# Optimization experiments

Measured on AMD Instinct MI355X. Metric: run time of the kernel, lower is better.

The kernel has to match this reference:

```python
import jax, jax.numpy as jnp
import numpy as np

D = 1024          # input_dim
H = 16            # num_heads
S = 2             # scalar
MAX_LEN = 2048
HEAD_DIM = D // H // S      # 32
DV = D // H                 # 64, value head dim
SCALING = (D // H) ** -0.5


def setup_inputs() -> dict:
    key = jax.random.key(0)
    k1, k2, k3, k4, k5, k6 = jax.random.split(key, 6)
    L, B = 2046, 4
    input_tensor = jax.random.normal(k1, (L, B, D), dtype=jnp.float32)
    # k_v_proj: Linear(MAX_LEN, MAX_LEN // S); bias exists but is unused in forward
    w_kv = jax.random.normal(k2, (MAX_LEN // S, MAX_LEN), dtype=jnp.float32) / np.sqrt(MAX_LEN)
    # q_proj: Linear(D, D // S)
    w_q = jax.random.normal(k3, (D // S, D), dtype=jnp.float32) / np.sqrt(D)
    b_q = jax.random.normal(k4, (D // S,), dtype=jnp.float32) * 0.01
    # out_proj: Linear(D, D)
    w_out = jax.random.normal(k5, (D, D), dtype=jnp.float32) / np.sqrt(D)
    b_out = jax.random.normal(k6, (D,), dtype=jnp.float32) * 0.01
    return {"input_tensor": input_tensor, "w_kv": w_kv, "w_q": w_q,
            "b_q": b_q, "w_out": w_out, "b_out": b_out}


def reference(input_tensor, w_kv, w_q, b_q, w_out, b_out):
    L, B, _ = input_tensor.shape
    P = L // S + 1                       # projected (low-rank) sequence length
    X = jnp.transpose(input_tensor, (1, 0, 2))        # [B, L, D]
    q = X @ w_q.T + b_q                                # [B, L, D/S]
    Wp = w_kv.T[:L, :P]                                # [L, P] sequence projection
    v = jnp.einsum('bld,lp->bdp', X, Wp)               # [B, D, P]
    k = jnp.einsum('blc,lp->bcp', q, Wp)               # [B, D/S, P]
    q = q * SCALING
    # q: b l (h d) -> b h l d
    qh = q.reshape(B, L, H, HEAD_DIM).transpose(0, 2, 1, 3)
    # k: b (d h) p -> b h d p   (d outer, h inner in the channel split)
    kh = k.reshape(B, HEAD_DIM, H, P).transpose(0, 2, 1, 3)
    # v: b (d h) p -> b h p d
    vh = v.reshape(B, DV, H, P).transpose(0, 2, 3, 1)
    attn = jnp.einsum('bhld,bhdp->bhlp', qh, kh)       # [B, H, L, P]
    attn = jax.nn.softmax(attn.astype(jnp.float32), axis=-1).astype(attn.dtype)
    out = jnp.einsum('bhlp,bhpd->bhld', attn, vh)      # [B, H, L, DV]
    # (b h) l d -> b l (d h): d outer, h inner in concat
    out = out.transpose(0, 2, 3, 1).reshape(B, L, D)
    out = out @ w_out.T + b_out                        # [B, L, D]
    return jnp.transpose(out, (1, 0, 2))               # [L, B, D]
```

## Files before the change

kernel.cpp:

```cpp
#include <hip/hip_runtime.h>
#include <hip/hip_bf16.h>

typedef long long i64;
typedef unsigned int uint;
using u16 = unsigned short;
using f32x4  = __attribute__((ext_vector_type(4))) float;
using bf16x8 = __attribute__((ext_vector_type(8))) short;
using u32x4  = __attribute__((ext_vector_type(4))) uint;
using u16x4  = __attribute__((ext_vector_type(4))) u16;

#define QSCALE 0.18033688011112042f

#if __has_builtin(__builtin_amdgcn_exp2f)
#define EXP2(x) __builtin_amdgcn_exp2f(x)
#else
#define EXP2(x) __builtin_exp2f(x)
#endif

__device__ __forceinline__ u16 f2b(float x) {
    uint u = __float_as_uint(x);
    return (u16)((u + 0x7FFFu + ((u >> 16) & 1u)) >> 16);
}
__device__ __forceinline__ uint cvt_pk_bf16(float lo, float hi) {
    uint r;
    asm("v_cvt_pk_bf16_f32 %0, %1, %2" : "=v"(r) : "v"(lo), "v"(hi));
    return r;
}

__global__ __launch_bounds__(256) void conv_pad(
    const float* __restrict__ src, u16* __restrict__ dst,
    int M_valid, int K_valid, int kshift, int s_row)
{
    i64 i = (i64)blockIdx.x * 256 + threadIdx.x;
    int m = (int)(i >> (kshift - 2));
    int k = ((int)(i & ((1 << (kshift - 2)) - 1))) << 2;
    u16x4 hv;
    #pragma unroll
    for (int j = 0; j < 4; ++j) {
        int kk = k + j;
        float x = (m < M_valid && kk < K_valid) ? src[(i64)m * s_row + kk] : 0.f;
        hv[j] = f2b(x);
    }
    *(u16x4*)(dst + ((i64)m << kshift) + k) = hv;
}

__global__ __launch_bounds__(256) void conv_wout_perm(
    const float* __restrict__ w, u16* __restrict__ dst)
{
    int i = blockIdx.x * 256 + threadIdx.x;
    int n = i >> 8, kp4 = (i & 255) << 2;
    u16x4 hv;
    #pragma unroll
    for (int j = 0; j < 4; ++j) {
        int kp = kp4 + j;
        hv[j] = f2b(w[((i64)n << 10) + ((kp & 63) << 4) + (kp >> 6)]);
    }
    *(u16x4*)(dst + ((i64)n << 10) + kp4) = hv;
}

__global__ __launch_bounds__(256) void build_kvA(
    const float* __restrict__ X, const float* __restrict__ qp,
    u16* __restrict__ dst)
{
    const int b = blockIdx.z, r0 = blockIdx.y * 64, l0 = blockIdx.x * 64;
    const int tid = threadIdx.x;
    __shared__ float ts[64][65];
    #pragma unroll
    for (int t = 0; t < 16; ++t) {
        int idx = t * 256 + tid;
        int ch = idx & 63, lr = idx >> 6;
        int lg = l0 + lr;
        float v = 0.f;
        if (lg < 2046) {
            if (r0 < 1024) v = X[(i64)lg * 4096 + b * 1024 + (r0 + ch)];
            else           v = qp[((i64)lg * 4 + b) * 512 + (r0 - 1024 + ch)];
        }
        ts[lr][ch] = v;
    }
    __syncthreads();
    #pragma unroll
    for (int t = 0; t < 16; ++t) {
        int idx = t * 256 + tid;
        int ll = idx & 63, rl = idx >> 6;
        dst[((i64)b * 1536 + r0 + rl) * 2048 + l0 + ll] = f2b(ts[ll][rl]);
    }
}

template<int MODE>
__global__ __launch_bounds__(256) void gemm_bf16(
    const u16* __restrict__ A, i64 a_bs,
    const u16* __restrict__ Bm,
    float* __restrict__ C, const float* __restrict__ bias,
    u16* __restrict__ x0, u16* __restrict__ x1,
    int Krow, int KT, int M_valid)
{
    __shared__ __align__(16) u16 As[4096], Bs[4096];
    const int tid = threadIdx.x, lane = tid & 63, w = tid >> 6;
    const int fr = lane & 15, g = lane >> 4;
    const int nb = blockIdx.x, mb = blockIdx.y, bz = blockIdx.z;

    const u16* src = (w < 2)
        ? (A + (i64)bz * a_bs + ((i64)mb * 128 + (w & 1) * 64) * Krow)
        : (Bm + ((i64)nb * 128 + (w & 1) * 64) * Krow);
    u16* dstb = (w < 2) ? As : Bs;
    const int R0 = (w & 1) * 64;
    const int lr = lane >> 2, lcg = lane & 3;

    f32x4 acc[4][4];
    #pragma unroll
    for (int i = 0; i < 4; ++i)
        #pragma unroll
        for (int j = 0; j < 4; ++j)
            acc[i][j] = (f32x4){0.f, 0.f, 0.f, 0.f};

    u32x4 st[4];
    #pragma unroll
    for (int it = 0; it < 4; ++it)
        st[it] = *(const u32x4*)(src + (i64)(it * 16 + lr) * Krow + lcg * 8);

    const int wr = (w >> 1) * 64, wc = (w & 1) * 64;

    for (int kt = 0; kt < KT; ++kt) {
        __syncthreads();
        #pragma unroll
        for (int it = 0; it < 4; ++it) {
            int R = R0 + it * 16 + lr;
            *(u32x4*)((char*)dstb + R * 64 + ((lcg ^ (R & 3)) << 4)) = st[it];
        }
        __syncthreads();
        if (kt + 1 < KT) {
            #pragma unroll
            for (int it = 0; it < 4; ++it)
                st[it] = *(const u32x4*)(src + (i64)(it * 16 + lr) * Krow
                                             + (kt + 1) * 32 + lcg * 8);
        }
        bf16x8 ah[4], bh[4];
        #pragma unroll
        for (int mi = 0; mi < 4; ++mi) {
            int rr = wr + mi * 16 + fr;
            ah[mi] = *(const bf16x8*)((const char*)As + rr * 64 + ((g * 16) ^ ((rr & 3) << 4)));
        }
        #pragma unroll
        for (int ni = 0; ni < 4; ++ni) {
            int rr = wc + ni * 16 + fr;
            bh[ni] = *(const bf16x8*)((const char*)Bs + rr * 64 + ((g * 16) ^ ((rr & 3) << 4)));
        }
        #pragma unroll
        for (int mi = 0; mi < 4; ++mi)
            #pragma unroll
            for (int ni = 0; ni < 4; ++ni)
                acc[mi][ni] = __builtin_amdgcn_mfma_f32_16x16x32_bf16(
                    ah[mi], bh[ni], acc[mi][ni], 0, 0, 0);
    }

    #pragma unroll
    for (int mi = 0; mi < 4; ++mi)
        #pragma unroll
        for (int ni = 0; ni < 4; ++ni) {
            int gm0 = mb * 128 + wr + mi * 16 + g * 4;
            int gn  = nb * 128 + wc + ni * 16 + fr;
            #pragma unroll
            for (int r = 0; r < 4; ++r) {
                int gm = gm0 + r;
                float val = acc[mi][ni][r];
                if (MODE == 0) {
                    val += bias[gn];
                    C[(i64)gm * 512 + gn] = val;
                    x0[(i64)gm * 512 + gn] = f2b(val * QSCALE);
                } else if (MODE == 1) {
                    if (gm < 1024) {
                        int e = gm >> 4, hh = gm & 15;
                        i64 s = ((i64)(bz * 16 + hh) * 64 + e) * 1024
                              + (gn & ~31) + (((gn >> 2) & 3) << 3)
                              + (gn & 3) + (((gn >> 4) & 1) << 2);
                        x1[s] = f2b(val);
                    } else {
                        int c2 = gm - 1024, d = c2 >> 4, hh = c2 & 15;
                        x0[((i64)(bz * 16 + hh) * 1024 + gn) * 32 + d] = f2b(val);
                    }
                } else {
                    if (gm < M_valid)
                        C[(i64)bz * 1024 + (i64)gm * 4096 + gn] = val + bias[gn];
                }
            }
        }
}

__global__ __launch_bounds__(256) void attn_mfma(
    const u16* __restrict__ qb, const u16* __restrict__ kT,
    const u16* __restrict__ vT, u16* __restrict__ attA)
{
    const int g0 = blockIdx.x;
    const int xcd = g0 & 7, sub = g0 >> 3;
    const int lblk = sub & 15;
    const int bh = xcd + ((sub >> 4) << 3);
    const int b = bh >> 4, h = bh & 15;
    const int tid = threadIdx.x, lane = tid & 63, w = tid >> 6;
    const int fr = lane & 15, g = lane >> 4;
    const int l0 = lblk * 128 + w * 32;

    __shared__ __align__(16) u16 kbuf[2][2560];
    __shared__ __align__(16) u16 vbuf[2][4608];

    bf16x8 aq[2];
    #pragma unroll
    for (int mf = 0; mf < 2; ++mf)
        aq[mf] = *(const bf16x8*)(qb + ((i64)((l0 + mf * 16 + fr) * 4 + b) * 512
                                        + h * 32 + g * 8));

    const f32x4 zf = {0.f, 0.f, 0.f, 0.f};

    const int sr = tid >> 2, sc = tid & 3;
    const u16* ksrc = kT + (i64)bh * 32768 + sr * 32 + sc * 8;
    char* kdst = (char*)&kbuf[0][0] + sr * 80 + sc * 16;
    const u16* vsrc = vT + (i64)bh * 65536 + (i64)sr * 1024 + sc * 8;
    char* vdst = (char*)&vbuf[0][0] + sr * 144 + sc * 16;

    *(u32x4*)kdst = *(const u32x4*)ksrc;
    *(u32x4*)vdst = *(const u32x4*)vsrc;
    *(u32x4*)(vdst + 64) = *(const u32x4*)(vsrc + 32);
    __syncthreads();

    float l_part[2] = {0.f, 0.f};
    f32x4 o[2][4];
    #pragma unroll
    for (int mf = 0; mf < 2; ++mf)
        #pragma unroll
        for (int nf = 0; nf < 4; ++nf)
            o[mf][nf] = zf;

    for (int t = 0; t < 16; ++t) {
        const int cur = t & 1;
        const int tn = (t < 15) ? t + 1 : 15;

        u32x4 knx  = *(const u32x4*)(ksrc + tn * 2048);
        u32x4 vnx0 = *(const u32x4*)(vsrc + tn * 64);
        u32x4 vnx1 = *(const u32x4*)(vsrc + tn * 64 + 32);

        const char* kc_ = (const char*)&kbuf[cur][0];
        f32x4 s[2][4];
        __builtin_amdgcn_s_setprio(1);
        #pragma unroll
        for (int nf = 0; nf < 4; ++nf) {
            bf16x8 ak = *(const bf16x8*)(kc_ + (nf * 16 + fr) * 80 + g * 16);
            s[0][nf] = __builtin_amdgcn_mfma_f32_16x16x32_bf16(ak, aq[0], zf, 0, 0, 0);
            s[1][nf] = __builtin_amdgcn_mfma_f32_16x16x32_bf16(ak, aq[1], zf, 0, 0, 0);
        }
        __builtin_amdgcn_s_setprio(0);

        u32x4 ppk[2][2];
        #pragma unroll
        for (int mf = 0; mf < 2; ++mf)
            #pragma unroll
            for (int nf = 0; nf < 4; ++nf) {
                float p_[4];
                #pragma unroll
                for (int r = 0; r < 4; ++r) p_[r] = EXP2(s[mf][nf][r]);
                l_part[mf] += (p_[0] + p_[1]) + (p_[2] + p_[3]);
                ppk[mf][nf >> 1][(nf & 1) * 2 + 0] = cvt_pk_bf16(p_[0], p_[1]);
                ppk[mf][nf >> 1][(nf & 1) * 2 + 1] = cvt_pk_bf16(p_[2], p_[3]);
            }

        {
            const int nb_ = cur ^ 1;
            *(u32x4*)(kdst + nb_ * 5120) = knx;
            *(u32x4*)(vdst + nb_ * 9216) = vnx0;
            *(u32x4*)(vdst + nb_ * 9216 + 64) = vnx1;
        }

        const char* vc_ = (const char*)&vbuf[cur][0];
        __builtin_amdgcn_s_setprio(1);
        #pragma unroll
        for (int ks = 0; ks < 2; ++ks) {
            bf16x8 ap0 = __builtin_bit_cast(bf16x8, ppk[0][ks]);
            bf16x8 ap1 = __builtin_bit_cast(bf16x8, ppk[1][ks]);
            #pragma unroll
            for (int nf = 0; nf < 4; ++nf) {
                bf16x8 bv = *(const bf16x8*)(vc_ + (nf * 16 + fr) * 144
                                                 + ks * 64 + g * 16);
                o[0][nf] = __builtin_amdgcn_mfma_f32_16x16x32_bf16(ap0, bv, o[0][nf], 0, 0, 0);
                o[1][nf] = __builtin_amdgcn_mfma_f32_16x16x32_bf16(ap1, bv, o[1][nf], 0, 0, 0);
            }
        }
        __builtin_amdgcn_s_setprio(0);

        __syncthreads();
    }

    #pragma unroll
    for (int mf = 0; mf < 2; ++mf) {
        l_part[mf] += __shfl_xor(l_part[mf], 16);
        l_part[mf] += __shfl_xor(l_part[mf], 32);
    }
    #pragma unroll
    for (int mf = 0; mf < 2; ++mf)
        #pragma unroll
        for (int r = 0; r < 4; ++r) {
            int l = l0 + mf * 16 + g * 4 + r;
            float tot = __shfl(l_part[mf], g * 4 + r);
            if (l < 2046) {
                float inv = 1.f / tot;
                #pragma unroll
                for (int nf = 0; nf < 4; ++nf)
                    attA[((i64)b * 2048 + l) * 1024 + h * 64 + nf * 16 + fr]
                        = f2b(o[mf][nf][r] * inv);
            }
        }
}

extern "C" void kernel_launch(void* const* d_in, const int* in_sizes, int n_in,
                              void* d_out, int out_size, void* d_ws, size_t ws_size,
                              hipStream_t stream) {
    const float* input = (const float*)d_in[0];
    const float* w_kv  = (const float*)d_in[1];
    const float* w_q   = (const float*)d_in[2];
    const float* b_q   = (const float*)d_in[3];
    const float* w_out = (const float*)d_in[4];
    const float* b_out = (const float*)d_in[5];
    float* out = (float*)d_out;

    char* W = (char*)d_ws;
    float* qp    = (float*)(W + 0);
    u16* Xb      = (u16*)(W + 16777216);
    u16* qb      = (u16*)(W + 33554432);
    u16* wq_b    = (u16*)(W + 41943040);
    u16* wkv_b   = (u16*)(W + 42991616);
    u16* wout_b  = (u16*)(W + 47185920);
    u16* kvA     = (u16*)(W + 49283072);
    u16* kT      = (u16*)(W + 74448896);
    u16* vT      = (u16*)(W + 78643200);
    u16* attA    = (u16*)(W + 87031808);

    dim3 blk(256);

    conv_pad<<<8192, blk, 0, stream>>>(input, Xb, 8184, 1024, 10, 1024);
    conv_pad<<<512,  blk, 0, stream>>>(w_q, wq_b, 512, 1024, 10, 1024);
    conv_pad<<<2048, blk, 0, stream>>>(w_kv, wkv_b, 1024, 2046, 11, 2048);
    conv_wout_perm<<<1024, blk, 0, stream>>>(w_out, wout_b);

    gemm_bf16<0><<<dim3(4, 64, 1), blk, 0, stream>>>(
        Xb, 0, wq_b, qp, b_q, qb, nullptr, 1024, 32, 8192);

    build_kvA<<<dim3(32, 24, 4), blk, 0, stream>>>(input, qp, kvA);

    gemm_bf16<1><<<dim3(8, 12, 4), blk, 0, stream>>>(
        kvA, (i64)1536 * 2048, wkv_b, nullptr, nullptr, kT, vT, 2048, 64, 1536);

    attn_mfma<<<dim3(1024), blk, 0, stream>>>(qb, kT, vT, attA);

    gemm_bf16<2><<<dim3(8, 16, 4), blk, 0, stream>>>(
        attA, (i64)2048 * 1024, wout_b, out, b_out, nullptr, nullptr, 1024, 32, 2046);
}
```

Baseline: 195.2 us.

## Double GEMM K-tile, add XCD-aware block mapping, drop fp32 q buffer

The GEMM kernel now loads a 64-wide K slice per iteration with an 8-way XOR swizzle, which halves the loop trip count and barrier count. Blocks are remapped from a 1D grid so that neighbouring tiles land on the same XCD, aiming for better L2 reuse. The fp32 q projection output is removed: q is stored once in bf16 without the scale, the scale is applied inside the attention exp2, and build_kvA reads bf16 X and q instead of fp32. Together these cut global traffic and loop overhead, at the cost of double the LDS per block and more staging registers, which may lower occupancy. They also feed k from bf16-rounded q instead of fp32 q, a small precision change.

```diff
diff --git a/kernel.cpp b/kernel.cpp
--- a/kernel.cpp
+++ b/kernel.cpp
@@ -21,6 +21,9 @@
     uint u = __float_as_uint(x);
     return (u16)((u + 0x7FFFu + ((u >> 16) & 1u)) >> 16);
 }
+__device__ __forceinline__ float b2f(u16 h) {
+    return __uint_as_float((uint)h << 16);
+}
 __device__ __forceinline__ uint cvt_pk_bf16(float lo, float hi) {
     uint r;
     asm("v_cvt_pk_bf16_f32 %0, %1, %2" : "=v"(r) : "v"(lo), "v"(hi));
@@ -59,7 +62,7 @@
 }
 
 __global__ __launch_bounds__(256) void build_kvA(
-    const float* __restrict__ X, const float* __restrict__ qp,
+    const u16* __restrict__ Xb, const u16* __restrict__ qu,
     u16* __restrict__ dst)
 {
     const int b = blockIdx.z, r0 = blockIdx.y * 64, l0 = blockIdx.x * 64;
@@ -72,8 +75,8 @@
         int lg = l0 + lr;
         float v = 0.f;
         if (lg < 2046) {
-            if (r0 < 1024) v = X[(i64)lg * 4096 + b * 1024 + (r0 + ch)];
-            else           v = qp[((i64)lg * 4 + b) * 512 + (r0 - 1024 + ch)];
+            if (r0 < 1024) v = b2f(Xb[((i64)lg * 4 + b) * 1024 + (r0 + ch)]);
+            else           v = b2f(qu[((i64)lg * 4 + b) * 512 + (r0 - 1024 + ch)]);
         }
         ts[lr][ch] = v;
     }
@@ -94,17 +97,25 @@
     u16* __restrict__ x0, u16* __restrict__ x1,
     int Krow, int KT, int M_valid)
 {
-    __shared__ __align__(16) u16 As[4096], Bs[4096];
+    __shared__ __align__(16) u16 As[8192], Bs[8192];
     const int tid = threadIdx.x, lane = tid & 63, w = tid >> 6;
     const int fr = lane & 15, g = lane >> 4;
-    const int nb = blockIdx.x, mb = blockIdx.y, bz = blockIdx.z;
+
+    const int fid = blockIdx.x;
+    const int xcd = fid & 7, s = fid >> 3;
+    int nb, mb, bz;
+    if (MODE == 0)      { nb = s & 3; mb = xcd * 8 + (s >> 2); bz = 0; }
+    else if (MODE == 1) { nb = s & 7; int pr = xcd * 6 + (s >> 3); bz = pr / 12; mb = pr % 12; }
+    else                { nb = s & 7; int pr = xcd * 8 + (s >> 3); bz = pr >> 4; mb = pr & 15; }
 
     const u16* src = (w < 2)
         ? (A + (i64)bz * a_bs + ((i64)mb * 128 + (w & 1) * 64) * Krow)
         : (Bm + ((i64)nb * 128 + (w & 1) * 64) * Krow);
     u16* dstb = (w < 2) ? As : Bs;
     const int R0 = (w & 1) * 64;
-    const int lr = lane >> 2, lcg = lane & 3;
+    const int lr8 = lane >> 3, lc8 = lane & 7;
+    const u16* src_lane = src + (i64)lr8 * Krow + ((lc8 ^ lr8) << 3);
+    char* wbase = (char*)dstb + (R0 + lr8) * 128 + lc8 * 16;
 
     f32x4 acc[4][4];
     #pragma unroll
@@ -113,44 +124,46 @@
         for (int j = 0; j < 4; ++j)
             acc[i][j] = (f32x4){0.f, 0.f, 0.f, 0.f};
 
-    u32x4 st[4];
-    #pragma unroll
-    for (int it = 0; it < 4; ++it)
-        st[it] = *(const u32x4*)(src + (i64)(it * 16 + lr) * Krow + lcg * 8);
+    u32x4 st[8];
+    #pragma unroll
+    for (int it = 0; it < 8; ++it)
+        st[it] = *(const u32x4*)(src_lane + (i64)(it * 8) * Krow);
 
     const int wr = (w >> 1) * 64, wc = (w & 1) * 64;
 
     for (int kt = 0; kt < KT; ++kt) {
         __syncthreads();
         #pragma unroll
-        for (int it = 0; it < 4; ++it) {
-            int R = R0 + it * 16 + lr;
-            *(u32x4*)((char*)dstb + R * 64 + ((lcg ^ (R & 3)) << 4)) = st[it];
-        }
+        for (int it = 0; it < 8; ++it)
+            *(u32x4*)(wbase + it * 1024) = st[it];
         __syncthreads();
         if (kt + 1 < KT) {
             #pragma unroll
-            for (int it = 0; it < 4; ++it)
-                st[it] = *(const u32x4*)(src + (i64)(it * 16 + lr) * Krow
-                                             + (kt + 1) * 32 + lcg * 8);
-        }
-        bf16x8 ah[4], bh[4];
-        #pragma unroll
-        for (int mi = 0; mi < 4; ++mi) {
-            int rr = wr + mi * 16 + fr;
-            ah[mi] = *(const bf16x8*)((const char*)As + rr * 64 + ((g * 16) ^ ((rr & 3) << 4)));
-        }
-        #pragma unroll
-        for (int ni = 0; ni < 4; ++ni) {
-            int rr = wc + ni * 16 + fr;
-            bh[ni] = *(const bf16x8*)((const char*)Bs + rr * 64 + ((g * 16) ^ ((rr & 3) << 4)));
-        }
-        #pragma unroll
-        for (int mi = 0; mi < 4; ++mi)
-            #pragma unroll
-            for (int ni = 0; ni < 4; ++ni)
-                acc[mi][ni] = __builtin_amdgcn_mfma_f32_16x16x32_bf16(
-                    ah[mi], bh[ni], acc[mi][ni], 0, 0, 0);
+            for (int it = 0; it < 8; ++it)
+                st[it] = *(const u32x4*)(src_lane + (i64)(it * 8) * Krow
+                                                  + (kt + 1) * 64);
+        }
+        #pragma unroll
+        for (int half = 0; half < 2; ++half) {
+            bf16x8 ah[4], bh[4];
+            const int co = ((half * 4 + g) ^ (fr & 7)) << 4;
+            #pragma unroll
+            for (int mi = 0; mi < 4; ++mi) {
+                int rr = wr + mi * 16 + fr;
+                ah[mi] = *(const bf16x8*)((const char*)As + rr * 128 + co);
+            }
+            #pragma unroll
+            for (int ni = 0; ni < 4; ++ni) {
+                int rr = wc + ni * 16 + fr;
+                bh[ni] = *(const bf16x8*)((const char*)Bs + rr * 128 + co);
+            }
+            #pragma unroll
+            for (int mi = 0; mi < 4; ++mi)
+                #pragma unroll
+                for (int ni = 0; ni < 4; ++ni)
+                    acc[mi][ni] = __builtin_amdgcn_mfma_f32_16x16x32_bf16(
+                        ah[mi], bh[ni], acc[mi][ni], 0, 0, 0);
+        }
     }
 
     #pragma unroll
@@ -164,16 +177,14 @@
                 int gm = gm0 + r;
                 float val = acc[mi][ni][r];
                 if (MODE == 0) {
-                    val += bias[gn];
-                    C[(i64)gm * 512 + gn] = val;
-                    x0[(i64)gm * 512 + gn] = f2b(val * QSCALE);
+                    x0[(i64)gm * 512 + gn] = f2b(val + bias[gn]);
                 } else if (MODE == 1) {
                     if (gm < 1024) {
                         int e = gm >> 4, hh = gm & 15;
-                        i64 s = ((i64)(bz * 16 + hh) * 64 + e) * 1024
-                              + (gn & ~31) + (((gn >> 2) & 3) << 3)
-                              + (gn & 3) + (((gn >> 4) & 1) << 2);
-                        x1[s] = f2b(val);
+                        i64 so = ((i64)(bz * 16 + hh) * 64 + e) * 1024
+                               + (gn & ~31) + (((gn >> 2) & 3) << 3)
+                               + (gn & 3) + (((gn >> 4) & 1) << 2);
+                        x1[so] = f2b(val);
                     } else {
                         int c2 = gm - 1024, d = c2 >> 4, hh = c2 & 15;
                         x0[((i64)(bz * 16 + hh) * 1024 + gn) * 32 + d] = f2b(val);
@@ -187,7 +198,7 @@
 }
 
 __global__ __launch_bounds__(256) void attn_mfma(
-    const u16* __restrict__ qb, const u16* __restrict__ kT,
+    const u16* __restrict__ qu, const u16* __restrict__ kT,
     const u16* __restrict__ vT, u16* __restrict__ attA)
 {
     const int g0 = blockIdx.x;
@@ -205,7 +216,7 @@
     bf16x8 aq[2];
     #pragma unroll
     for (int mf = 0; mf < 2; ++mf)
-        aq[mf] = *(const bf16x8*)(qb + ((i64)((l0 + mf * 16 + fr) * 4 + b) * 512
+        aq[mf] = *(const bf16x8*)(qu + ((i64)((l0 + mf * 16 + fr) * 4 + b) * 512
                                         + h * 32 + g * 8));
 
     const f32x4 zf = {0.f, 0.f, 0.f, 0.f};
@@ -255,7 +266,7 @@
             for (int nf = 0; nf < 4; ++nf) {
                 float p_[4];
                 #pragma unroll
-                for (int r = 0; r < 4; ++r) p_[r] = EXP2(s[mf][nf][r]);
+                for (int r = 0; r < 4; ++r) p_[r] = EXP2(QSCALE * s[mf][nf][r]);
                 l_part[mf] += (p_[0] + p_[1]) + (p_[2] + p_[3]);
                 ppk[mf][nf >> 1][(nf & 1) * 2 + 0] = cvt_pk_bf16(p_[0], p_[1]);
                 ppk[mf][nf >> 1][(nf & 1) * 2 + 1] = cvt_pk_bf16(p_[2], p_[3]);
@@ -320,9 +331,8 @@
     float* out = (float*)d_out;
 
     char* W = (char*)d_ws;
-    float* qp    = (float*)(W + 0);
     u16* Xb      = (u16*)(W + 16777216);
-    u16* qb      = (u16*)(W + 33554432);
+    u16* qu      = (u16*)(W + 33554432);
     u16* wq_b    = (u16*)(W + 41943040);
     u16* wkv_b   = (u16*)(W + 42991616);
     u16* wout_b  = (u16*)(W + 47185920);
@@ -338,16 +348,16 @@
     conv_pad<<<2048, blk, 0, stream>>>(w_kv, wkv_b, 1024, 2046, 11, 2048);
     conv_wout_perm<<<1024, blk, 0, stream>>>(w_out, wout_b);
 
-    gemm_bf16<0><<<dim3(4, 64, 1), blk, 0, stream>>>(
-        Xb, 0, wq_b, qp, b_q, qb, nullptr, 1024, 32, 8192);
-
-    build_kvA<<<dim3(32, 24, 4), blk, 0, stream>>>(input, qp, kvA);
-
-    gemm_bf16<1><<<dim3(8, 12, 4), blk, 0, stream>>>(
-        kvA, (i64)1536 * 2048, wkv_b, nullptr, nullptr, kT, vT, 2048, 64, 1536);
-
-    attn_mfma<<<dim3(1024), blk, 0, stream>>>(qb, kT, vT, attA);
-
-    gemm_bf16<2><<<dim3(8, 16, 4), blk, 0, stream>>>(
-        attA, (i64)2048 * 1024, wout_b, out, b_out, nullptr, nullptr, 1024, 32, 2046);
-}
+    gemm_bf16<0><<<dim3(256), blk, 0, stream>>>(
+        Xb, 0, wq_b, nullptr, b_q, qu, nullptr, 1024, 16, 8192);
+
+    build_kvA<<<dim3(32, 24, 4), blk, 0, stream>>>(Xb, qu, kvA);
+
+    gemm_bf16<1><<<dim3(384), blk, 0, stream>>>(
+        kvA, (i64)1536 * 2048, wkv_b, nullptr, nullptr, kT, vT, 2048, 32, 1536);
+
+    attn_mfma<<<dim3(1024), blk, 0, stream>>>(qu, kT, vT, attA);
+
+    gemm_bf16<2><<<dim3(512), blk, 0, stream>>>(
+        attA, (i64)2048 * 1024, wout_b, out, b_out, nullptr, nullptr, 1024, 16, 2046);
+}
```

After: 184.7 us. 1.06x faster.
